# Kernel optimization log

Hardware: AMD Instinct MI355X
Metric: run time of the kernel (lower is better)

The kernel has to match this reference:

```python
import jax, jax.numpy as jnp
import numpy as np

EMBED = 768
HEADS = 12
HEAD_DIM = EMBED // HEADS  # 64


def setup_inputs() -> dict:
    key = jax.random.key(0)
    ks = jax.random.split(key, 9)
    d = HEAD_DIM
    s = 1.0 / np.sqrt(d)
    return {
        "x": jax.random.normal(ks[0], (8, 1024, EMBED), dtype=jnp.float32),
        "ln_w": jnp.ones((EMBED,), dtype=jnp.float32),
        "ln_b": jnp.zeros((EMBED,), dtype=jnp.float32),
        "Wq": jax.random.uniform(ks[1], (d, d), jnp.float32, -s, s),
        "bq": jax.random.uniform(ks[2], (d,), jnp.float32, -s, s),
        "Wk": jax.random.uniform(ks[3], (d, d), jnp.float32, -s, s),
        "bk": jax.random.uniform(ks[4], (d,), jnp.float32, -s, s),
        "Wv": jax.random.uniform(ks[5], (d, d), jnp.float32, -s, s),
        "bv": jax.random.uniform(ks[6], (d,), jnp.float32, -s, s),
    }


def reference(x, ln_w, ln_b, Wq, bq, Wk, bk, Wv, bv):
    bs, n, e = x.shape
    # LayerNorm over last dim (eps matches torch default 1e-5)
    mu = jnp.mean(x, axis=-1, keepdims=True)
    var = jnp.mean(jnp.square(x - mu), axis=-1, keepdims=True)
    xn = (x - mu) / jnp.sqrt(var + 1e-5) * ln_w + ln_b
    # Raw view split (NOT transpose split): [bs, n, E] -> [bs, H, n, d]
    xh = xn.reshape(bs, HEADS, n, HEAD_DIM)
    # Linear layers (torch Linear: y = x @ W.T + b)
    q = jnp.einsum("bhnd,ed->bhne", xh, Wq) + bq
    k = jnp.einsum("bhnd,ed->bhne", xh, Wk) + bk
    v = jnp.einsum("bhnd,ed->bhne", xh, Wv) + bv
    # Unusual: softmax FIRST, then divide by sqrt(d)
    scores = jnp.einsum("bhqd,bhkd->bhqk", q, k)
    attn = jax.nn.softmax(scores, axis=-1) / jnp.sqrt(jnp.float32(HEAD_DIM))
    feature = jnp.einsum("bhqk,bhkd->bhqd", attn, v)
    return feature.reshape(bs, n, e)
```

## Files before the change

### kernel.cpp

```cpp
#include <hip/hip_runtime.h>

#define EMBED 768
#define HEADS 12
#define HD 64
#define SEQ 1024
#define BS 8
#define NROWS (BS * HEADS * SEQ)
#define XP 72
#define PLP 40

typedef _Float16 f16;
typedef f16 f16x4 __attribute__((ext_vector_type(4)));
typedef f16 f16x8 __attribute__((ext_vector_type(8)));
typedef float f32x4 __attribute__((ext_vector_type(4)));

__global__ __launch_bounds__(256) void k_lnstats(const float* __restrict__ x,
                                                 const float* __restrict__ Wq,
                                                 const float* __restrict__ Wk,
                                                 const float* __restrict__ Wv,
                                                 float* __restrict__ mu_out,
                                                 float* __restrict__ rs_out,
                                                 f16* __restrict__ wf) {
    const int w = threadIdx.x >> 6;
    const int lane = threadIdx.x & 63;
    const int row = blockIdx.x * 4 + w;
    const float4* xr = (const float4*)(x + (long)row * EMBED);
    float s = 0.f, sq = 0.f;
#pragma unroll
    for (int kk = 0; kk < 3; ++kk) {
        float4 v = xr[lane + kk * 64];
        s += v.x + v.y + v.z + v.w;
        sq += v.x * v.x + v.y * v.y + v.z * v.z + v.w * v.w;
    }
#pragma unroll
    for (int off = 32; off; off >>= 1) {
        s += __shfl_xor(s, off, 64);
        sq += __shfl_xor(sq, off, 64);
    }
    if (lane == 0) {
        float mu = s * (1.f / EMBED);
        float var = sq * (1.f / EMBED) - mu * mu;
        mu_out[row] = mu;
        rs_out[row] = rsqrtf(var + 1e-5f);
    }
    if (blockIdx.x < 3) {
        const float* W = (blockIdx.x == 0) ? Wq : (blockIdx.x == 1) ? Wk : Wv;
        f16* dst = wf + (long)blockIdx.x * 4096;
        const int t = threadIdx.x;
#pragma unroll
        for (int i = 0; i < 2; ++i) {
            const int o = t * 2 + i;
            const int nt = o >> 7, half = (o >> 6) & 1, lp = o & 63;
            const int qd = lp >> 4, l16 = lp & 15;
            const float* src = W + (nt * 16 + l16) * 64 + half * 32 + qd * 8;
            float4 v0 = *(const float4*)src, v1 = *(const float4*)(src + 4);
            f16x8 h = {(f16)v0.x, (f16)v0.y, (f16)v0.z, (f16)v0.w,
                       (f16)v1.x, (f16)v1.y, (f16)v1.z, (f16)v1.w};
            *(f16x8*)(dst + o * 8) = h;
        }
    }
}

__global__ __launch_bounds__(256) void k_qkv(
    const float* __restrict__ x, const float* __restrict__ lw, const float* __restrict__ lb,
    const f16* __restrict__ wf,
    const float* __restrict__ bq, const float* __restrict__ bk, const float* __restrict__ bv,
    const float* __restrict__ mu, const float* __restrict__ rs,
    f16* __restrict__ qo, f16* __restrict__ ko, f16* __restrict__ vo) {
    __shared__ __align__(16) f16 xh[64 * XP];
    const int t = threadIdx.x;
    const unsigned r0 = (unsigned)blockIdx.x * 64;
    const int bh = (int)(r0 >> 10);
    const int seq0 = (int)(r0 & 1023);
    const int tile0 = seq0 >> 5;

    {
        const unsigned fb = r0 * 64u + (unsigned)t * 16u;
        const unsigned xrow = fb / EMBED;
        const unsigned c0 = fb % EMBED;
        const float m_ = mu[xrow], s_ = rs[xrow];
        const int lrow = (t * 16) >> 6, lcol = (t * 16) & 63;
        f16* dst = &xh[lrow * XP + lcol];
        const float4* xp = (const float4*)(x + fb);
        const float4* wp = (const float4*)(lw + c0);
        const float4* bp = (const float4*)(lb + c0);
#pragma unroll
        for (int j = 0; j < 4; ++j) {
            float4 xv = xp[j], wv = wp[j], bv2 = bp[j];
            f16x4 h = {(f16)((xv.x - m_) * s_ * wv.x + bv2.x), (f16)((xv.y - m_) * s_ * wv.y + bv2.y),
                       (f16)((xv.z - m_) * s_ * wv.z + bv2.z), (f16)((xv.w - m_) * s_ * wv.w + bv2.w)};
            *(f16x4*)(dst + j * 4) = h;
        }
    }
    __syncthreads();

    const int lane = t & 63, w = t >> 6, l16 = lane & 15, quad = lane >> 4;
    f16x8 a0 = *(const f16x8*)&xh[(w * 16 + l16) * XP + quad * 8];
    f16x8 a1 = *(const f16x8*)&xh[(w * 16 + l16) * XP + 32 + quad * 8];
    const float* Bs[3] = {bq, bk, bv};

#pragma unroll
    for (int m = 0; m < 3; ++m) {
        const f16* wfm = wf + (long)m * 4096 + lane * 8;
        f32x4 acc[4];
#pragma unroll
        for (int nt = 0; nt < 4; ++nt) {
            f16x8 b0 = *(const f16x8*)(wfm + (nt * 2 + 0) * 512);
            f16x8 b1 = *(const f16x8*)(wfm + (nt * 2 + 1) * 512);
            f32x4 a = {0.f, 0.f, 0.f, 0.f};
            a = __builtin_amdgcn_mfma_f32_16x16x32_f16(a0, b0, a, 0, 0, 0);
            a = __builtin_amdgcn_mfma_f32_16x16x32_f16(a1, b1, a, 0, 0, 0);
            const float bias = Bs[m][nt * 16 + l16];
#pragma unroll
            for (int rg = 0; rg < 4; ++rg) a[rg] += bias;
            acc[nt] = a;
        }

        __syncthreads();
        if (m < 2) {
#pragma unroll
            for (int nt = 0; nt < 4; ++nt)
#pragma unroll
                for (int rg = 0; rg < 4; ++rg)
                    xh[(w * 16 + quad * 4 + rg) * XP + nt * 16 + l16] = (f16)acc[nt][rg];
        } else {
#pragma unroll
            for (int nt = 0; nt < 4; ++nt) {
                f16x4 h = {(f16)acc[nt][0], (f16)acc[nt][1], (f16)acc[nt][2], (f16)acc[nt][3]};
                *(f16x4*)&xh[(nt * 16 + l16) * XP + w * 16 + quad * 4] = h;
            }
        }
        __syncthreads();
        if (m == 0) {
#pragma unroll
            for (int c = t; c < 512; c += 256) {
                const int row = c >> 3, c8 = (c & 7) * 8;
                *(f16x8*)(qo + ((long)r0 + row) * 64 + c8) = *(const f16x8*)&xh[row * XP + c8];
            }
        } else if (m == 1) {
            f16* kb = ko + ((long)bh << 16) + (long)tile0 * 2048;
#pragma unroll
            for (int c = t; c < 512; c += 256) {
                const int tl = c >> 8, chunk = (c >> 6) & 3, qd = (c >> 4) & 3, l16s = c & 15;
                const int row = tl * 32 + (chunk >> 1) * 16 + l16s;
                const int col = (chunk & 1) * 32 + qd * 8;
                *(f16x8*)(kb + (long)c * 8) = *(const f16x8*)&xh[row * XP + col];
            }
        } else {
            f16* vb = vo + ((long)bh << 16) + (long)tile0 * 2048;
#pragma unroll
            for (int c = t; c < 512; c += 256) {
                const int tl = c >> 8, nt = (c >> 6) & 3, qd = (c >> 4) & 3, l16d = c & 15;
                *(f16x8*)(vb + (long)c * 8) = *(const f16x8*)&xh[(nt * 16 + l16d) * XP + tl * 32 + qd * 8];
            }
        }
    }
}

__global__ __launch_bounds__(256) void k_attn(const f16* __restrict__ q,
                                              const f16* __restrict__ k,
                                              const f16* __restrict__ vt,
                                              float* __restrict__ out) {
    __shared__ __align__(16) f16 pl[4][32 * PLP];
    const int t = threadIdx.x;
    const int w = t >> 6, lane = t & 63, l16 = lane & 15, quad = lane >> 4;
    const int bh = blockIdx.x;
    const int q0 = blockIdx.y * 128 + w * 32;
    const long hb = (long)bh * SEQ;
    const f16* kp0 = k + ((long)bh << 16) + lane * 8;
    const f16* vp0 = vt + ((long)bh << 16) + lane * 8;

    f16x8 qf[2][2];
#pragma unroll
    for (int mt = 0; mt < 2; ++mt) {
        const f16* qp = q + (hb + q0 + mt * 16 + l16) * 64 + quad * 8;
        qf[mt][0] = *(const f16x8*)qp;
        qf[mt][1] = *(const f16x8*)(qp + 32);
    }
    f32x4 o[2][4];
    f32x4 ls[2];
#pragma unroll
    for (int mt = 0; mt < 2; ++mt) {
        ls[mt] = (f32x4){0.f, 0.f, 0.f, 0.f};
#pragma unroll
        for (int nt = 0; nt < 4; ++nt) o[mt][nt] = (f32x4){0.f, 0.f, 0.f, 0.f};
    }
    f16x8 one;
#pragma unroll
    for (int j = 0; j < 8; ++j) one[j] = (f16)1.0f;

#define LOADK(kt, kf)                                  \
    {                                                  \
        const f16* kp = kp0 + (kt) * 2048;             \
        kf[0] = *(const f16x8*)kp;                     \
        kf[1] = *(const f16x8*)(kp + 512);             \
        kf[2] = *(const f16x8*)(kp + 1024);            \
        kf[3] = *(const f16x8*)(kp + 1536);            \
    }
#define LOADV(kt, vf)                                  \
    {                                                  \
        const f16* vp = vp0 + (kt) * 2048;             \
        vf[0] = *(const f16x8*)vp;                     \
        vf[1] = *(const f16x8*)(vp + 512);             \
        vf[2] = *(const f16x8*)(vp + 1024);            \
        vf[3] = *(const f16x8*)(vp + 1536);            \
    }

    f16x8 ka[4], va[4], kb[4], vb[4];
    LOADK(0, ka);
    LOADV(0, va);

    auto body = [&](const f16x8* kf, const f16x8* vf) {
        f32x4 s[2][2];
#pragma unroll
        for (int mt = 0; mt < 2; ++mt) {
            f32x4 a = {0.f, 0.f, 0.f, 0.f};
            a = __builtin_amdgcn_mfma_f32_16x16x32_f16(qf[mt][0], kf[0], a, 0, 0, 0);
            a = __builtin_amdgcn_mfma_f32_16x16x32_f16(qf[mt][1], kf[1], a, 0, 0, 0);
            s[mt][0] = a;
            f32x4 b = {0.f, 0.f, 0.f, 0.f};
            b = __builtin_amdgcn_mfma_f32_16x16x32_f16(qf[mt][0], kf[2], b, 0, 0, 0);
            b = __builtin_amdgcn_mfma_f32_16x16x32_f16(qf[mt][1], kf[3], b, 0, 0, 0);
            s[mt][1] = b;
        }
#pragma unroll
        for (int mt = 0; mt < 2; ++mt)
#pragma unroll
            for (int ct = 0; ct < 2; ++ct)
#pragma unroll
                for (int rg = 0; rg < 4; ++rg) {
                    float p = __expf(s[mt][ct][rg] - 14.f);
                    pl[w][(mt * 16 + quad * 4 + rg) * PLP + ct * 16 + l16] = (f16)p;
                }
        f16x8 pf0 = *(const f16x8*)&pl[w][l16 * PLP + quad * 8];
        f16x8 pf1 = *(const f16x8*)&pl[w][(16 + l16) * PLP + quad * 8];
        ls[0] = __builtin_amdgcn_mfma_f32_16x16x32_f16(pf0, one, ls[0], 0, 0, 0);
        ls[1] = __builtin_amdgcn_mfma_f32_16x16x32_f16(pf1, one, ls[1], 0, 0, 0);
#pragma unroll
        for (int nt = 0; nt < 4; ++nt) {
            o[0][nt] = __builtin_amdgcn_mfma_f32_16x16x32_f16(pf0, vf[nt], o[0][nt], 0, 0, 0);
            o[1][nt] = __builtin_amdgcn_mfma_f32_16x16x32_f16(pf1, vf[nt], o[1][nt], 0, 0, 0);
        }
    };

    for (int kt = 0; kt < SEQ / 32; kt += 2) {
        LOADK(kt + 1, kb);
        LOADV(kt + 1, vb);
        body(ka, va);
        const int kn = (kt + 2 < SEQ / 32) ? kt + 2 : SEQ / 32 - 1;
        LOADK(kn, ka);
        LOADV(kn, va);
        body(kb, vb);
    }
#undef LOADK
#undef LOADV

#pragma unroll
    for (int mt = 0; mt < 2; ++mt) {
        float inv[4];
#pragma unroll
        for (int rg = 0; rg < 4; ++rg) inv[rg] = 1.f / (ls[mt][rg] * 8.0f);
#pragma unroll
        for (int nt = 0; nt < 4; ++nt) {
            float* op = out + (hb + q0 + mt * 16 + quad * 4) * 64 + nt * 16 + l16;
#pragma unroll
            for (int rg = 0; rg < 4; ++rg) op[(long)rg * 64] = o[mt][nt][rg] * inv[rg];
        }
    }
}

extern "C" void kernel_launch(void* const* d_in, const int* in_sizes, int n_in,
                              void* d_out, int out_size, void* d_ws, size_t ws_size,
                              hipStream_t stream) {
    const float* x = (const float*)d_in[0];
    const float* lw = (const float*)d_in[1];
    const float* lb = (const float*)d_in[2];
    const float* Wq = (const float*)d_in[3];
    const float* bq = (const float*)d_in[4];
    const float* Wk = (const float*)d_in[5];
    const float* bk = (const float*)d_in[6];
    const float* Wv = (const float*)d_in[7];
    const float* bv = (const float*)d_in[8];
    float* out = (float*)d_out;

    char* ws = (char*)d_ws;
    float* mu = (float*)ws;
    float* rs = (float*)(ws + 32768);
    f16* wfr = (f16*)(ws + 65536);
    f16* qo = (f16*)(ws + 98304);
    f16* ko = qo + (long)NROWS * 64;
    f16* vo = ko + (long)NROWS * 64;

    k_lnstats<<<2048, 256, 0, stream>>>(x, Wq, Wk, Wv, mu, rs, wfr);
    k_qkv<<<NROWS / 64, 256, 0, stream>>>(x, lw, lb, wfr, bq, bk, bv, mu, rs, qo, ko, vo);
    k_attn<<<dim3(BS * HEADS, SEQ / 128), 256, 0, stream>>>(qo, ko, vo, out);
}
```

Before: 142.6 us.

## Permute key order for packed P conversion and double qkv rows per block

The attention kernel now starts the score accumulators at -14, which removes a subtract before each exp. It packs pairs of exp values into half precision with one cvt_pkrtz and one store, interleaving the two 16-key column tiles in the P buffer. The V layout written by the qkv kernel is permuted to match, so the PV product stays correct; this adds gather-style shared reads on the V side. The qkv kernel also handles 128 rows per block with two shared subtiles, halving the grid and reusing the weight fragments across both subtiles, at the cost of more registers and shared memory per block.

```diff
diff --git a/kernel.cpp b/kernel.cpp
--- a/kernel.cpp
+++ b/kernel.cpp
@@ -67,20 +67,21 @@
     const float* __restrict__ bq, const float* __restrict__ bk, const float* __restrict__ bv,
     const float* __restrict__ mu, const float* __restrict__ rs,
     f16* __restrict__ qo, f16* __restrict__ ko, f16* __restrict__ vo) {
-    __shared__ __align__(16) f16 xh[64 * XP];
+    __shared__ __align__(16) f16 xh[2][64 * XP];
     const int t = threadIdx.x;
-    const unsigned r0 = (unsigned)blockIdx.x * 64;
+    const unsigned r0 = (unsigned)blockIdx.x * 128;
     const int bh = (int)(r0 >> 10);
     const int seq0 = (int)(r0 & 1023);
     const int tile0 = seq0 >> 5;
 
-    {
-        const unsigned fb = r0 * 64u + (unsigned)t * 16u;
+#pragma unroll
+    for (int st = 0; st < 2; ++st) {
+        const unsigned fb = (r0 + st * 64u) * 64u + (unsigned)t * 16u;
         const unsigned xrow = fb / EMBED;
         const unsigned c0 = fb % EMBED;
         const float m_ = mu[xrow], s_ = rs[xrow];
         const int lrow = (t * 16) >> 6, lcol = (t * 16) & 63;
-        f16* dst = &xh[lrow * XP + lcol];
+        f16* dst = &xh[st][lrow * XP + lcol];
         const float4* xp = (const float4*)(x + fb);
         const float4* wp = (const float4*)(lw + c0);
         const float4* bp = (const float4*)(lb + c0);
@@ -95,63 +96,86 @@
     __syncthreads();
 
     const int lane = t & 63, w = t >> 6, l16 = lane & 15, quad = lane >> 4;
-    f16x8 a0 = *(const f16x8*)&xh[(w * 16 + l16) * XP + quad * 8];
-    f16x8 a1 = *(const f16x8*)&xh[(w * 16 + l16) * XP + 32 + quad * 8];
+    f16x8 a[2][2];
+#pragma unroll
+    for (int st = 0; st < 2; ++st) {
+        a[st][0] = *(const f16x8*)&xh[st][(w * 16 + l16) * XP + quad * 8];
+        a[st][1] = *(const f16x8*)&xh[st][(w * 16 + l16) * XP + 32 + quad * 8];
+    }
     const float* Bs[3] = {bq, bk, bv};
 
 #pragma unroll
     for (int m = 0; m < 3; ++m) {
         const f16* wfm = wf + (long)m * 4096 + lane * 8;
-        f32x4 acc[4];
+        f32x4 acc[2][4];
 #pragma unroll
         for (int nt = 0; nt < 4; ++nt) {
             f16x8 b0 = *(const f16x8*)(wfm + (nt * 2 + 0) * 512);
             f16x8 b1 = *(const f16x8*)(wfm + (nt * 2 + 1) * 512);
-            f32x4 a = {0.f, 0.f, 0.f, 0.f};
-            a = __builtin_amdgcn_mfma_f32_16x16x32_f16(a0, b0, a, 0, 0, 0);
-            a = __builtin_amdgcn_mfma_f32_16x16x32_f16(a1, b1, a, 0, 0, 0);
             const float bias = Bs[m][nt * 16 + l16];
 #pragma unroll
-            for (int rg = 0; rg < 4; ++rg) a[rg] += bias;
-            acc[nt] = a;
+            for (int st = 0; st < 2; ++st) {
+                f32x4 a_ = {0.f, 0.f, 0.f, 0.f};
+                a_ = __builtin_amdgcn_mfma_f32_16x16x32_f16(a[st][0], b0, a_, 0, 0, 0);
+                a_ = __builtin_amdgcn_mfma_f32_16x16x32_f16(a[st][1], b1, a_, 0, 0, 0);
+#pragma unroll
+                for (int rg = 0; rg < 4; ++rg) a_[rg] += bias;
+                acc[st][nt] = a_;
+            }
         }
 
         __syncthreads();
         if (m < 2) {
 #pragma unroll
-            for (int nt = 0; nt < 4; ++nt)
-#pragma unroll
-                for (int rg = 0; rg < 4; ++rg)
-                    xh[(w * 16 + quad * 4 + rg) * XP + nt * 16 + l16] = (f16)acc[nt][rg];
+            for (int st = 0; st < 2; ++st)
+#pragma unroll
+                for (int nt = 0; nt < 4; ++nt)
+#pragma unroll
+                    for (int rg = 0; rg < 4; ++rg)
+                        xh[st][(w * 16 + quad * 4 + rg) * XP + nt * 16 + l16] = (f16)acc[st][nt][rg];
         } else {
 #pragma unroll
-            for (int nt = 0; nt < 4; ++nt) {
-                f16x4 h = {(f16)acc[nt][0], (f16)acc[nt][1], (f16)acc[nt][2], (f16)acc[nt][3]};
-                *(f16x4*)&xh[(nt * 16 + l16) * XP + w * 16 + quad * 4] = h;
-            }
+            for (int st = 0; st < 2; ++st)
+#pragma unroll
+                for (int nt = 0; nt < 4; ++nt) {
+                    f16x4 h = {(f16)acc[st][nt][0], (f16)acc[st][nt][1], (f16)acc[st][nt][2], (f16)acc[st][nt][3]};
+                    *(f16x4*)&xh[st][(nt * 16 + l16) * XP + w * 16 + quad * 4] = h;
+                }
         }
         __syncthreads();
         if (m == 0) {
 #pragma unroll
-            for (int c = t; c < 512; c += 256) {
-                const int row = c >> 3, c8 = (c & 7) * 8;
-                *(f16x8*)(qo + ((long)r0 + row) * 64 + c8) = *(const f16x8*)&xh[row * XP + c8];
-            }
+            for (int st = 0; st < 2; ++st)
+#pragma unroll
+                for (int c = t; c < 512; c += 256) {
+                    const int row = c >> 3, c8 = (c & 7) * 8;
+                    *(f16x8*)(qo + ((long)r0 + st * 64 + row) * 64 + c8) = *(const f16x8*)&xh[st][row * XP + c8];
+                }
         } else if (m == 1) {
-            f16* kb = ko + ((long)bh << 16) + (long)tile0 * 2048;
-#pragma unroll
-            for (int c = t; c < 512; c += 256) {
-                const int tl = c >> 8, chunk = (c >> 6) & 3, qd = (c >> 4) & 3, l16s = c & 15;
-                const int row = tl * 32 + (chunk >> 1) * 16 + l16s;
-                const int col = (chunk & 1) * 32 + qd * 8;
-                *(f16x8*)(kb + (long)c * 8) = *(const f16x8*)&xh[row * XP + col];
+#pragma unroll
+            for (int st = 0; st < 2; ++st) {
+                f16* kb = ko + ((long)bh << 16) + (long)(tile0 + st * 2) * 2048;
+#pragma unroll
+                for (int c = t; c < 512; c += 256) {
+                    const int tl = c >> 8, chunk = (c >> 6) & 3, qd = (c >> 4) & 3, l16s = c & 15;
+                    const int row = tl * 32 + (chunk >> 1) * 16 + l16s;
+                    const int col = (chunk & 1) * 32 + qd * 8;
+                    *(f16x8*)(kb + (long)c * 8) = *(const f16x8*)&xh[st][row * XP + col];
+                }
             }
         } else {
-            f16* vb = vo + ((long)bh << 16) + (long)tile0 * 2048;
-#pragma unroll
-            for (int c = t; c < 512; c += 256) {
-                const int tl = c >> 8, nt = (c >> 6) & 3, qd = (c >> 4) & 3, l16d = c & 15;
-                *(f16x8*)(vb + (long)c * 8) = *(const f16x8*)&xh[(nt * 16 + l16d) * XP + tl * 32 + qd * 8];
+#pragma unroll
+            for (int st = 0; st < 2; ++st) {
+                f16* vb = vo + ((long)bh << 16) + (long)(tile0 + st * 2) * 2048;
+#pragma unroll
+                for (int c = t; c < 512; c += 256) {
+                    const int tl = c >> 8, nt = (c >> 6) & 3, qd = (c >> 4) & 3, l16d = c & 15;
+                    const f16* base = &xh[st][(nt * 16 + l16d) * XP + tl * 32 + qd * 4];
+                    f16x4 lo = *(const f16x4*)base;
+                    f16x4 hi = *(const f16x4*)(base + 16);
+                    f16x8 o8 = {lo[0], hi[0], lo[1], hi[1], lo[2], hi[2], lo[3], hi[3]};
+                    *(f16x8*)(vb + (long)c * 8) = o8;
+                }
             }
         }
     }
@@ -188,6 +212,7 @@
     f16x8 one;
 #pragma unroll
     for (int j = 0; j < 8; ++j) one[j] = (f16)1.0f;
+    const f32x4 m14 = {-14.f, -14.f, -14.f, -14.f};
 
 #define LOADK(kt, kf)                                  \
     {                                                  \
@@ -214,11 +239,11 @@
         f32x4 s[2][2];
 #pragma unroll
         for (int mt = 0; mt < 2; ++mt) {
-            f32x4 a = {0.f, 0.f, 0.f, 0.f};
+            f32x4 a = m14;
             a = __builtin_amdgcn_mfma_f32_16x16x32_f16(qf[mt][0], kf[0], a, 0, 0, 0);
             a = __builtin_amdgcn_mfma_f32_16x16x32_f16(qf[mt][1], kf[1], a, 0, 0, 0);
             s[mt][0] = a;
-            f32x4 b = {0.f, 0.f, 0.f, 0.f};
+            f32x4 b = m14;
             b = __builtin_amdgcn_mfma_f32_16x16x32_f16(qf[mt][0], kf[2], b, 0, 0, 0);
             b = __builtin_amdgcn_mfma_f32_16x16x32_f16(qf[mt][1], kf[3], b, 0, 0, 0);
             s[mt][1] = b;
@@ -226,12 +251,12 @@
 #pragma unroll
         for (int mt = 0; mt < 2; ++mt)
 #pragma unroll
-            for (int ct = 0; ct < 2; ++ct)
-#pragma unroll
-                for (int rg = 0; rg < 4; ++rg) {
-                    float p = __expf(s[mt][ct][rg] - 14.f);
-                    pl[w][(mt * 16 + quad * 4 + rg) * PLP + ct * 16 + l16] = (f16)p;
-                }
+            for (int rg = 0; rg < 4; ++rg) {
+                float e0 = __expf(s[mt][0][rg]);
+                float e1 = __expf(s[mt][1][rg]);
+                auto pk = __builtin_amdgcn_cvt_pkrtz(e0, e1);
+                *(decltype(pk)*)&pl[w][(mt * 16 + quad * 4 + rg) * PLP + l16 * 2] = pk;
+            }
         f16x8 pf0 = *(const f16x8*)&pl[w][l16 * PLP + quad * 8];
         f16x8 pf1 = *(const f16x8*)&pl[w][(16 + l16) * PLP + quad * 8];
         ls[0] = __builtin_amdgcn_mfma_f32_16x16x32_f16(pf0, one, ls[0], 0, 0, 0);
@@ -292,6 +317,6 @@
     f16* vo = ko + (long)NROWS * 64;
 
     k_lnstats<<<2048, 256, 0, stream>>>(x, Wq, Wk, Wv, mu, rs, wfr);
-    k_qkv<<<NROWS / 64, 256, 0, stream>>>(x, lw, lb, wfr, bq, bk, bv, mu, rs, qo, ko, vo);
+    k_qkv<<<NROWS / 128, 256, 0, stream>>>(x, lw, lb, wfr, bq, bk, bv, mu, rs, qo, ko, vo);
     k_attn<<<dim3(BS * HEADS, SEQ / 128), 256, 0, stream>>>(qo, ko, vo, out);
 }
```

Result: faster. 139.6 us (-2.1%).
